# Performance work log

Measured on AMD Instinct MI355X. Metric: run time of the kernel, lower is better.

Reference implementation:

```python
import jax, jax.numpy as jnp
import numpy as np

N = 524288
L, T, F = 24, 1 << 19, 2          # levels, hashmap size per level, features per level
BASE_RES, MAX_RES = 16, 2048
PRIMES = np.array([1, 2654435761, 805459861], dtype=np.uint32)
# per-level resolutions, geometric growth (instant-ngp)
_b = np.exp((np.log(MAX_RES) - np.log(BASE_RES)) / (L - 1))
RES = np.floor(BASE_RES * _b ** np.arange(L)).astype(np.float32)  # [L]
CORNERS = np.stack(np.meshgrid(*[[0, 1]] * 3, indexing='ij'), -1).reshape(8, 3)  # [8,3]


def hash_encode(points, table):
    # points in [-1,1]^3 (bb_sides=2.0) -> [0,1]^3
    x = (points + 1.0) * 0.5
    pos = x[:, None, :] * jnp.asarray(RES)[None, :, None]      # [N,L,3]
    pos0 = jnp.floor(pos)
    w = pos - pos0                                             # [N,L,3] trilinear weights
    c = pos0[:, :, None, :].astype(jnp.uint32) + jnp.asarray(CORNERS, jnp.uint32)[None, None]  # [N,L,8,3]
    p = jnp.asarray(PRIMES)
    idx = ((c[..., 0] * p[0]) ^ (c[..., 1] * p[1]) ^ (c[..., 2] * p[2])) & jnp.uint32(T - 1)   # [N,L,8]
    feats = table[jnp.arange(L)[None, :, None], idx]           # [N,L,8,F]
    cb = jnp.asarray(CORNERS, jnp.float32)[None, None]         # [1,1,8,3]
    wts = jnp.prod(cb * w[:, :, None, :] + (1.0 - cb) * (1.0 - w[:, :, None, :]), axis=-1)  # [N,L,8]
    out = jnp.sum(feats * wts[..., None], axis=2)              # [N,L,F]
    return out.reshape(points.shape[0], L * F)                 # [N,48]


def sh3_encode(d):
    # real spherical harmonics, degree 3 -> 9 coefficients
    x, y, z = d[:, 0], d[:, 1], d[:, 2]
    return jnp.stack([
        jnp.full_like(x, 0.28209479177387814),
        -0.48860251190291987 * y,
        0.48860251190291987 * z,
        -0.48860251190291987 * x,
        1.0925484305920792 * x * y,
        -1.0925484305920792 * y * z,
        0.31539156525252005 * (3.0 * z * z - 1.0),
        -1.0925484305920792 * x * z,
        0.5462742152960396 * (x * x - y * y),
    ], axis=-1)                                                # [N,9]


def _gelu(x):
    return jax.nn.gelu(x, approximate=False)


def reference(samples_3d, samples_dirs, hash_table,
              fw0, fb0, fw1, fb1, fw2, fb2, fw3, fb3,
              rw0, rb0, rw1, rb1, rw2, rb2, iter_nr):
    enc = hash_encode(samples_3d, hash_table)                  # [N,48]
    dirs_enc = jax.lax.stop_gradient(sh3_encode(samples_dirs)) # no-grad dir encoding
    # mlp_feat_and_density: 48->64->64->64->65, GELU hidden, last linear
    h = _gelu(enc @ fw0 + fb0)
    h = _gelu(h @ fw1 + fb1)
    h = _gelu(h @ fw2 + fb2)
    fad = h @ fw3 + fb3                                        # [N,65]
    density = jax.nn.softplus(fad[:, 0:1])                     # [N,1]
    feat_rgb = _gelu(fad[:, 1:65])                             # [N,64]
    x = jnp.concatenate([feat_rgb, dirs_enc], axis=1)          # [N,73]
    # mlp_rgb: 73->64->64->3, GELU hidden, last linear
    h = _gelu(x @ rw0 + rb0)
    h = _gelu(h @ rw1 + rb1)
    rgb = jax.nn.sigmoid(h @ rw2 + rb2)                        # [N,3]
    return rgb, density


def setup_inputs():
    key = jax.random.key(0)
    ks = jax.random.split(key, 24)
    pts = jax.random.uniform(ks[0], (N, 3), minval=-1.0, maxval=1.0)
    d = jax.random.normal(ks[1], (N, 3))
    d = d / jnp.linalg.norm(d, axis=-1, keepdims=True)
    table = jax.random.uniform(ks[2], (L, T, F), minval=-1e-4, maxval=1e-4)

    def lin(k, fi, fo):
        k1, k2 = jax.random.split(k)
        s = 1.0 / np.sqrt(fi)
        return (jax.random.uniform(k1, (fi, fo), minval=-s, maxval=s),
                jax.random.uniform(k2, (fo,), minval=-s, maxval=s))

    inp = {"samples_3d": pts, "samples_dirs": d, "hash_table": table}
    i = 3
    for j, (fi, fo) in enumerate([(48, 64), (64, 64), (64, 64), (64, 65)]):
        w, b = lin(ks[i], fi, fo); inp[f"fw{j}"] = w; inp[f"fb{j}"] = b; i += 1
    for j, (fi, fo) in enumerate([(73, 64), (64, 64), (64, 3)]):
        w, b = lin(ks[i], fi, fo); inp[f"rw{j}"] = w; inp[f"rb{j}"] = b; i += 1
    inp["iter_nr"] = 0
    return inp
```

## Files before the change

### kernel.cpp

```cpp
#include <hip/hip_runtime.h>
#include <math.h>

#define LVL 24
#define TMASK ((1u << 19) - 1u)

typedef short short8 __attribute__((ext_vector_type(8)));
typedef float floatx4 __attribute__((ext_vector_type(4)));

struct ResParams { float r[LVL]; };

__device__ __forceinline__ float bf2f(unsigned short b) {
  union { unsigned u; float f; } t; t.u = ((unsigned)b) << 16; return t.f;
}
__device__ __forceinline__ unsigned f2bf(float f) {
  union { float f; unsigned u; } t; t.f = f;
  unsigned u = t.u;
  u += 0x7FFFu + ((u >> 16) & 1u);
  return u >> 16;
}
__device__ __forceinline__ float geluf(float x) {
  float a = fabsf(x) * 0.7071067811865476f;
  float t = __builtin_amdgcn_rcpf(fmaf(0.3275911f, a, 1.0f));
  float p = fmaf(t, 1.061405429f, -1.453152027f);
  p = fmaf(t, p, 1.421413741f);
  p = fmaf(t, p, -0.284496736f);
  p = fmaf(t, p, 0.254829592f);
  float er = 1.0f - p * t * __expf(-a * a);
  return 0.5f * x * (1.0f + copysignf(er, x));
}
__device__ __forceinline__ floatx4 mfma16(short8 a, short8 b, floatx4 c) {
  return __builtin_amdgcn_mfma_f32_16x16x32_bf16(a, b, c, 0, 0, 0);
}

#define L0_W 0
#define L1_W 4096
#define L2_W 8192
#define L3_W 12288
#define L4_W 17408
#define L5_W 23552
#define L6_W 27648
#define L0_F 0
#define L1_F 512
#define L2_F 1024
#define L3_F 1536
#define L4_F 2176
#define L5_F 2944
#define L6_F 3456

__device__ void prepF(const float* w, short* dst, int K, int NOUT, int KCH, int CBS) {
  int total = KCH * CBS * 64 * 8;
  for (int i = threadIdx.x; i < total; i += 256) {
    int j = i & 7;
    int lane = (i >> 3) & 63;
    int cbc = i >> 9;
    int cb = cbc % CBS;
    int c  = cbc / CBS;
    int n = cb * 16 + (lane & 15);
    int k = c * 32 + (lane >> 4) * 8 + j;
    short v = 0;
    if (k < K && n < NOUT) v = (short)f2bf(w[k * NOUT + n]);
    dst[i] = v;
  }
}
__global__ __launch_bounds__(256) void prep_all(
    const float* __restrict__ fw0, const float* __restrict__ fb0,
    const float* __restrict__ fw1, const float* __restrict__ fb1,
    const float* __restrict__ fw2, const float* __restrict__ fb2,
    const float* __restrict__ fw3, const float* __restrict__ fb3,
    const float* __restrict__ rw0, const float* __restrict__ rb0,
    const float* __restrict__ rw1, const float* __restrict__ rb1,
    const float* __restrict__ rw2, const float* __restrict__ rb2,
    short* __restrict__ Wimg, float* __restrict__ Bimg,
    const float* __restrict__ tbl, unsigned* __restrict__ tblq, int nent,
    int pack_on)
{
  int b = blockIdx.x, tid = threadIdx.x;
  if (b >= 8) {
    if (!pack_on) return;
    int g = (b - 8) * 256 + tid;
    int stride = (gridDim.x - 8) * 256;
    const float4* t4 = (const float4*)tbl;
    uint2* q2 = (uint2*)tblq;
    int n4 = nent >> 1;
    for (int e = g; e < n4; e += stride) {
      float4 v = t4[e];
      uint2 o;
      o.x = f2bf(v.x) | (f2bf(v.y) << 16);
      o.y = f2bf(v.z) | (f2bf(v.w) << 16);
      q2[e] = o;
    }
    return;
  }
  switch (b) {
    case 0: prepF(fw0, Wimg + L0_W, 48, 64, 2, 4); break;
    case 1: prepF(fw1, Wimg + L1_W, 64, 64, 2, 4); break;
    case 2: prepF(fw2, Wimg + L2_W, 64, 64, 2, 4); break;
    case 3: prepF(fw3, Wimg + L3_W, 64, 65, 2, 5); break;
    case 4: prepF(rw0, Wimg + L4_W, 73, 64, 3, 4); break;
    case 5: prepF(rw1, Wimg + L5_W, 64, 64, 2, 4); break;
    case 6: prepF(rw2, Wimg + L6_W, 64,  3, 2, 1); break;
    case 7:
      if (tid < 64) {
        Bimg[tid]       = fb0[tid];
        Bimg[64 + tid]  = fb1[tid];
        Bimg[128 + tid] = fb2[tid];
        Bimg[272 + tid] = rb0[tid];
        Bimg[336 + tid] = rb1[tid];
      }
      if (tid < 80) Bimg[192 + tid] = (tid < 65) ? fb3[tid] : 0.0f;
      if (tid < 16) Bimg[400 + tid] = (tid < 3) ? rb2[tid] : 0.0f;
      break;
  }
}

template<bool PACKED>
__global__ __launch_bounds__(256) void hash_encode_k(
    const float* __restrict__ pts, const float* __restrict__ tbl,
    const unsigned* __restrict__ tblq, unsigned* __restrict__ enc2,
    int N, ResParams rp)
{
  __shared__ float pbuf[4][192];
  int bid  = blockIdx.x;
  int wave = threadIdx.x >> 6;
  int lane = threadIdx.x & 63;
  int l    = bid >> 11;
  int p0   = ((bid & 2047) << 8) + wave * 64;
  int p    = p0 + lane;
  float res = rp.r[l];

  {
    const float* pf = pts + (size_t)p0 * 3;
    pbuf[wave][lane]       = pf[lane];
    pbuf[wave][64 + lane]  = pf[64 + lane];
    pbuf[wave][128 + lane] = pf[128 + lane];
  }
  float x = (pbuf[wave][lane * 3 + 0] + 1.0f) * 0.5f * res;
  float y = (pbuf[wave][lane * 3 + 1] + 1.0f) * 0.5f * res;
  float z = (pbuf[wave][lane * 3 + 2] + 1.0f) * 0.5f * res;

  float fx = floorf(x), fy = floorf(y), fz = floorf(z);
  float w0 = x - fx, w1 = y - fy, w2 = z - fz;
  unsigned c0 = (unsigned)fx, c1 = (unsigned)fy, c2 = (unsigned)fz;
  unsigned hy0 = c1 * 2654435761u, hy1 = hy0 + 2654435761u;
  unsigned hz0 = c2 * 805459861u,  hz1 = hz0 + 805459861u;
  bool ceven = ((c0 & 1u) == 0u);

  const unsigned* tq = PACKED ? (tblq + ((size_t)l << 19)) : nullptr;
  const float*    tf = PACKED ? nullptr : (tbl + ((size_t)l << 20));

  float f0 = 0.f, f1 = 0.f;
  #pragma unroll
  for (int yz = 0; yz < 4; ++yz) {
    unsigned hyz = ((yz & 2) ? hy1 : hy0) ^ ((yz & 1) ? hz1 : hz0);
    float wyz = ((yz & 2) ? w1 : 1.f - w1) * ((yz & 1) ? w2 : 1.f - w2);
    unsigned h0 = (c0 ^ hyz) & TMASK;
    unsigned h1 = ((c0 + 1u) ^ hyz) & TMASK;
    float e00, e01, e10, e11;
    if constexpr (PACKED) {
      unsigned v0, v1;
      if (ceven) {
        uint2 v = *(const uint2*)(tq + (h0 & ~1u));
        v0 = (h0 & 1u) ? v.y : v.x;
        v1 = (h0 & 1u) ? v.x : v.y;
      } else {
        v0 = tq[h0];
        v1 = tq[h1];
      }
      e00 = bf2f((unsigned short)(v0 & 0xffffu)); e01 = bf2f((unsigned short)(v0 >> 16));
      e10 = bf2f((unsigned short)(v1 & 0xffffu)); e11 = bf2f((unsigned short)(v1 >> 16));
    } else {
      if (ceven) {
        float4 v = *(const float4*)(tf + 2u * (h0 & ~1u));
        if (h0 & 1u) { e00 = v.z; e01 = v.w; e10 = v.x; e11 = v.y; }
        else         { e00 = v.x; e01 = v.y; e10 = v.z; e11 = v.w; }
      } else {
        float2 a = *(const float2*)(tf + 2u * h0);
        float2 b = *(const float2*)(tf + 2u * h1);
        e00 = a.x; e01 = a.y; e10 = b.x; e11 = b.y;
      }
    }
    float wa = (1.f - w0) * wyz, wb = w0 * wyz;
    f0 += wa * e00 + wb * e10;
    f1 += wa * e01 + wb * e11;
  }
  enc2[l * N + p] = f2bf(f0) | (f2bf(f1) << 16);
}

template<int NF>
__device__ __forceinline__ void loadB(const short8* Wf, int lane, short8* B) {
  #pragma unroll
  for (int i = 0; i < NF; ++i) B[i] = Wf[i * 64 + lane];
}
template<int KCH, int CBS>
__device__ __forceinline__ void mfma_layer(const short* At, const short8* B,
                                           int m, int quad,
                                           floatx4* acc0, floatx4* acc1) {
  #pragma unroll
  for (int cb = 0; cb < CBS; ++cb) {
    acc0[cb] = (floatx4){0.f, 0.f, 0.f, 0.f};
    acc1[cb] = (floatx4){0.f, 0.f, 0.f, 0.f};
  }
  #pragma unroll
  for (int c = 0; c < KCH; ++c) {
    short8 a0 = *(const short8*)(At + m * 104 + c * 32 + quad * 8);
    short8 a1 = *(const short8*)(At + (16 + m) * 104 + c * 32 + quad * 8);
    #pragma unroll
    for (int cb = 0; cb < CBS; ++cb) {
      acc0[cb] = mfma16(a0, B[c * CBS + cb], acc0[cb]);
      acc1[cb] = mfma16(a1, B[c * CBS + cb], acc1[cb]);
    }
  }
}

__global__ __launch_bounds__(256, 4) void mlp_g(
    const float* __restrict__ dirs,
    const unsigned* __restrict__ enc2,
    const short* __restrict__ Wimg, const float* __restrict__ Bimg,
    float* __restrict__ outp, int Nrows)
{
  __shared__ __align__(16) short Atile[4 * 32 * 104];
  __shared__ __align__(16) float Blds[416];

  const int tid  = threadIdx.x;
  const int wave = tid >> 6;
  const int lane = tid & 63;
  const int m    = lane & 15;
  const int quad = lane >> 4;
  const int row0 = blockIdx.x * 128 + wave * 32;
  short* At = Atile + wave * (32 * 104);
  const short8* Wf = (const short8*)Wimg;

  short8 B[12];
  loadB<8>(Wf + L0_F, lane, B);

  if (tid < 104) ((float4*)Blds)[tid] = ((const float4*)Bimg)[tid];

  if (lane < 32) {
    int row = row0 + lane;
    float dx = dirs[row * 3 + 0];
    float dy = dirs[row * 3 + 1];
    float dz = dirs[row * 3 + 2];
    short8 z8 = {0, 0, 0, 0, 0, 0, 0, 0};
    short8 s07;
    s07[0] = (short)f2bf(0.28209479177387814f);
    s07[1] = (short)f2bf(-0.48860251190291987f * dy);
    s07[2] = (short)f2bf(0.48860251190291987f * dz);
    s07[3] = (short)f2bf(-0.48860251190291987f * dx);
    s07[4] = (short)f2bf(1.0925484305920792f * dx * dy);
    s07[5] = (short)f2bf(-1.0925484305920792f * dy * dz);
    s07[6] = (short)f2bf(0.31539156525252005f * (3.0f * dz * dz - 1.0f));
    s07[7] = (short)f2bf(-1.0925484305920792f * dx * dz);
    short8 s8v = {0, 0, 0, 0, 0, 0, 0, 0};
    s8v[0] = (short)f2bf(0.5462742152960396f * (dx * dx - dy * dy));
    short* rb = At + lane * 104;
    *(short8*)(rb + 48) = z8;
    *(short8*)(rb + 56) = z8;
    *(short8*)(rb + 64) = s07;
    *(short8*)(rb + 72) = s8v;
    *(short8*)(rb + 80) = z8;
    *(short8*)(rb + 88) = z8;
    *(short8*)(rb + 96) = z8;
  }

  for (int i = lane; i < 32 * LVL; i += 64) {
    int l = i >> 5;
    int r = i & 31;
    unsigned v = enc2[l * Nrows + row0 + r];
    *(unsigned*)(At + r * 104 + 2 * l) = v;
  }

  __syncthreads();

  floatx4 acc0[5], acc1[5];

#define EPI_GELU(BOFF)                                                        \
  _Pragma("unroll")                                                           \
  for (int cb = 0; cb < 4; ++cb) {                                            \
    float bc = Blds[(BOFF) + cb * 16 + m];                                    \
    _Pragma("unroll")                                                         \
    for (int r = 0; r < 4; ++r) {                                             \
      At[(quad * 4 + r) * 104 + cb * 16 + m]      = (short)f2bf(geluf(acc0[cb][r] + bc)); \
      At[(16 + quad * 4 + r) * 104 + cb * 16 + m] = (short)f2bf(geluf(acc1[cb][r] + bc)); \
    }                                                                         \
  }

  mfma_layer<2, 4>(At, B, m, quad, acc0, acc1);
  loadB<8>(Wf + L1_F, lane, B);
  EPI_GELU(0)
  mfma_layer<2, 4>(At, B, m, quad, acc0, acc1);
  loadB<8>(Wf + L2_F, lane, B);
  EPI_GELU(64)
  mfma_layer<2, 4>(At, B, m, quad, acc0, acc1);
  loadB<10>(Wf + L3_F, lane, B);
  EPI_GELU(128)
  mfma_layer<2, 5>(At, B, m, quad, acc0, acc1);
  loadB<12>(Wf + L4_F, lane, B);
  #pragma unroll
  for (int cb = 0; cb < 5; ++cb) {
    int col = cb * 16 + m;
    float bc = Blds[192 + col];
    #pragma unroll
    for (int r = 0; r < 4; ++r) {
      #pragma unroll
      for (int t = 0; t < 2; ++t) {
        float v = (t ? acc1[cb][r] : acc0[cb][r]) + bc;
        int row = t * 16 + quad * 4 + r;
        if (col == 0) {
          float d = (v > 15.f) ? v : __logf(1.0f + __expf(v));
          outp[3 * Nrows + row0 + row] = d;
        } else if (col <= 64) {
          At[row * 104 + (col - 1)] = (short)f2bf(geluf(v));
        }
      }
    }
  }
  mfma_layer<3, 4>(At, B, m, quad, acc0, acc1);
  loadB<8>(Wf + L5_F, lane, B);
  EPI_GELU(272)
  mfma_layer<2, 4>(At, B, m, quad, acc0, acc1);
  loadB<2>(Wf + L6_F, lane, B);
  EPI_GELU(336)
  mfma_layer<2, 1>(At, B, m, quad, acc0, acc1);
  {
    float bc = Blds[400 + m];
    #pragma unroll
    for (int r = 0; r < 4; ++r) {
      #pragma unroll
      for (int t = 0; t < 2; ++t) {
        float v = (t ? acc1[0][r] : acc0[0][r]) + bc;
        float s = __builtin_amdgcn_rcpf(1.0f + __expf(-v));
        int row = t * 16 + quad * 4 + r;
        if (m < 3) outp[(row0 + row) * 3 + m] = s;
      }
    }
  }
#undef EPI_GELU
}

#define W0_OFF 0
#define W1_OFF 4608
#define W2_OFF 9216
#define W3_OFF 13824
#define R0_OFF 0
#define R1_OFF 6656
#define R2_OFF 11264

template<int K, int NOUT, int NROWS, int STRIDE>
__device__ void stageW(const float* w, short* dst, int tid) {
  for (int i = tid; i < NROWS * STRIDE; i += 256) {
    int n = i / STRIDE;
    int k = i - n * STRIDE;
    short v = 0;
    if (n < NOUT && k < K) v = (short)f2bf(w[k * NOUT + n]);
    dst[i] = v;
  }
}
template<int NOUT, int NPAD>
__device__ void stageB(const float* b, float* dst, int tid) {
  for (int i = tid; i < NPAD; i += 256) dst[i] = (i < NOUT) ? b[i] : 0.0f;
}
template<int KCH, int CBS, int WSTRIDE>
__device__ __forceinline__ void run_layer(const short* At, const short* Wb,
                                          int m, int quad, floatx4* acc) {
  #pragma unroll
  for (int cb = 0; cb < CBS; ++cb) acc[cb] = (floatx4){0.f, 0.f, 0.f, 0.f};
  #pragma unroll
  for (int c = 0; c < KCH; ++c) {
    short8 a = *(const short8*)(At + m * 104 + c * 32 + quad * 8);
    #pragma unroll
    for (int cb = 0; cb < CBS; ++cb) {
      short8 b = *(const short8*)(Wb + (cb * 16 + m) * WSTRIDE + c * 32 + quad * 8);
      acc[cb] = mfma16(a, b, acc[cb]);
    }
  }
}

__global__ __launch_bounds__(256, 2) void nerf_fused(
    const float* __restrict__ pts,
    const float* __restrict__ dirs,
    const float* __restrict__ tbl,
    const float* __restrict__ fw0, const float* __restrict__ fb0,
    const float* __restrict__ fw1, const float* __restrict__ fb1,
    const float* __restrict__ fw2, const float* __restrict__ fb2,
    const float* __restrict__ fw3, const float* __restrict__ fb3,
    const float* __restrict__ rw0, const float* __restrict__ rb0,
    const float* __restrict__ rw1, const float* __restrict__ rb1,
    const float* __restrict__ rw2, const float* __restrict__ rb2,
    float* __restrict__ outp, int Nrows, ResParams rp)
{
  __shared__ __align__(16) short Wlds[19584];
  __shared__ __align__(16) float Blds[272];
  __shared__ __align__(16) short Atile[4 * 16 * 104];

  const int tid  = threadIdx.x;
  const int wave = tid >> 6;
  const int lane = tid & 63;
  const int m    = lane & 15;
  const int quad = lane >> 4;
  const int row0 = blockIdx.x * 64 + wave * 16;
  short* At = Atile + wave * (16 * 104);

  stageW<48, 64, 64, 72>(fw0, Wlds + W0_OFF, tid);
  stageW<64, 64, 64, 72>(fw1, Wlds + W1_OFF, tid);
  stageW<64, 64, 64, 72>(fw2, Wlds + W2_OFF, tid);
  stageW<64, 65, 80, 72>(fw3, Wlds + W3_OFF, tid);
  stageB<64, 64>(fb0, Blds + 0,   tid);
  stageB<64, 64>(fb1, Blds + 64,  tid);
  stageB<64, 64>(fb2, Blds + 128, tid);
  stageB<65, 80>(fb3, Blds + 192, tid);

  if (lane < 16) {
    int row = row0 + lane;
    float dx = dirs[row * 3 + 0];
    float dy = dirs[row * 3 + 1];
    float dz = dirs[row * 3 + 2];
    short8 z8 = {0, 0, 0, 0, 0, 0, 0, 0};
    short8 s07;
    s07[0] = (short)f2bf(0.28209479177387814f);
    s07[1] = (short)f2bf(-0.48860251190291987f * dy);
    s07[2] = (short)f2bf(0.48860251190291987f * dz);
    s07[3] = (short)f2bf(-0.48860251190291987f * dx);
    s07[4] = (short)f2bf(1.0925484305920792f * dx * dy);
    s07[5] = (short)f2bf(-1.0925484305920792f * dy * dz);
    s07[6] = (short)f2bf(0.31539156525252005f * (3.0f * dz * dz - 1.0f));
    s07[7] = (short)f2bf(-1.0925484305920792f * dx * dz);
    short8 s8v = {0, 0, 0, 0, 0, 0, 0, 0};
    s8v[0] = (short)f2bf(0.5462742152960396f * (dx * dx - dy * dy));
    short* rb = At + lane * 104;
    *(short8*)(rb + 48) = z8;
    *(short8*)(rb + 56) = z8;
    *(short8*)(rb + 64) = s07;
    *(short8*)(rb + 72) = s8v;
    *(short8*)(rb + 80) = z8;
    *(short8*)(rb + 88) = z8;
    *(short8*)(rb + 96) = z8;
  }

  for (int t = lane; t < 16 * LVL; t += 64) {
    int r = t / LVL;
    int l = t - r * LVL;
    int row = row0 + r;
    float res = rp.r[l];
    float x = (pts[row * 3 + 0] + 1.0f) * 0.5f * res;
    float y = (pts[row * 3 + 1] + 1.0f) * 0.5f * res;
    float z = (pts[row * 3 + 2] + 1.0f) * 0.5f * res;
    float fx = floorf(x), fy = floorf(y), fz = floorf(z);
    float w0 = x - fx, w1 = y - fy, w2 = z - fz;
    unsigned c0 = (unsigned)fx, c1 = (unsigned)fy, c2 = (unsigned)fz;
    unsigned ha0 = c0, hb0 = c0 + 1u;
    unsigned ha1 = c1 * 2654435761u, hb1 = ha1 + 2654435761u;
    unsigned ha2 = c2 * 805459861u,  hb2 = ha2 + 805459861u;
    const float* tb = tbl + ((size_t)l << 20);
    float f0 = 0.f, f1 = 0.f;
    #pragma unroll
    for (int i = 0; i < 8; ++i) {
      unsigned h = ((i & 4) ? hb0 : ha0) ^ ((i & 2) ? hb1 : ha1) ^ ((i & 1) ? hb2 : ha2);
      float wt = ((i & 4) ? w0 : 1.f - w0) * ((i & 2) ? w1 : 1.f - w1) * ((i & 1) ? w2 : 1.f - w2);
      float2 fv = *(const float2*)(tb + 2u * (h & TMASK));
      f0 += wt * fv.x;
      f1 += wt * fv.y;
    }
    unsigned pk = f2bf(f0) | (f2bf(f1) << 16);
    *(unsigned*)(At + r * 104 + 2 * l) = pk;
  }

  __syncthreads();

  floatx4 acc[5];

  run_layer<2, 4, 72>(At, Wlds + W0_OFF, m, quad, acc);
  #pragma unroll
  for (int cb = 0; cb < 4; ++cb) {
    float bc = Blds[0 + cb * 16 + m];
    #pragma unroll
    for (int r = 0; r < 4; ++r) {
      float v = geluf(acc[cb][r] + bc);
      At[(quad * 4 + r) * 104 + cb * 16 + m] = (short)f2bf(v);
    }
  }
  run_layer<2, 4, 72>(At, Wlds + W1_OFF, m, quad, acc);
  #pragma unroll
  for (int cb = 0; cb < 4; ++cb) {
    float bc = Blds[64 + cb * 16 + m];
    #pragma unroll
    for (int r = 0; r < 4; ++r) {
      float v = geluf(acc[cb][r] + bc);
      At[(quad * 4 + r) * 104 + cb * 16 + m] = (short)f2bf(v);
    }
  }
  run_layer<2, 4, 72>(At, Wlds + W2_OFF, m, quad, acc);
  #pragma unroll
  for (int cb = 0; cb < 4; ++cb) {
    float bc = Blds[128 + cb * 16 + m];
    #pragma unroll
    for (int r = 0; r < 4; ++r) {
      float v = geluf(acc[cb][r] + bc);
      At[(quad * 4 + r) * 104 + cb * 16 + m] = (short)f2bf(v);
    }
  }
  run_layer<2, 5, 72>(At, Wlds + W3_OFF, m, quad, acc);
  #pragma unroll
  for (int cb = 0; cb < 5; ++cb) {
    int col = cb * 16 + m;
    float bc = Blds[192 + col];
    #pragma unroll
    for (int r = 0; r < 4; ++r) {
      float v = acc[cb][r] + bc;
      int row = quad * 4 + r;
      if (col == 0) {
        float d = (v > 15.f) ? v : __logf(1.0f + __expf(v));
        outp[3 * Nrows + row0 + row] = d;
      } else if (col <= 64) {
        At[row * 104 + (col - 1)] = (short)f2bf(geluf(v));
      }
    }
  }

  __syncthreads();

  stageW<73, 64, 64, 104>(rw0, Wlds + R0_OFF, tid);
  stageW<64, 64, 64,  72>(rw1, Wlds + R1_OFF, tid);
  stageW<64,  3, 16,  72>(rw2, Wlds + R2_OFF, tid);
  stageB<64, 64>(rb0, Blds + 0,   tid);
  stageB<64, 64>(rb1, Blds + 64,  tid);
  stageB< 3, 16>(rb2, Blds + 128, tid);

  __syncthreads();

  run_layer<3, 4, 104>(At, Wlds + R0_OFF, m, quad, acc);
  #pragma unroll
  for (int cb = 0; cb < 4; ++cb) {
    float bc = Blds[0 + cb * 16 + m];
    #pragma unroll
    for (int r = 0; r < 4; ++r) {
      float v = geluf(acc[cb][r] + bc);
      At[(quad * 4 + r) * 104 + cb * 16 + m] = (short)f2bf(v);
    }
  }
  run_layer<2, 4, 72>(At, Wlds + R1_OFF, m, quad, acc);
  #pragma unroll
  for (int cb = 0; cb < 4; ++cb) {
    float bc = Blds[64 + cb * 16 + m];
    #pragma unroll
    for (int r = 0; r < 4; ++r) {
      float v = geluf(acc[cb][r] + bc);
      At[(quad * 4 + r) * 104 + cb * 16 + m] = (short)f2bf(v);
    }
  }
  run_layer<2, 1, 72>(At, Wlds + R2_OFF, m, quad, acc);
  {
    float bc = Blds[128 + m];
    #pragma unroll
    for (int r = 0; r < 4; ++r) {
      float v = acc[0][r] + bc;
      float s = __builtin_amdgcn_rcpf(1.0f + __expf(-v));
      if (m < 3) outp[(row0 + quad * 4 + r) * 3 + m] = s;
    }
  }
}

extern "C" void kernel_launch(void* const* d_in, const int* in_sizes, int n_in,
                              void* d_out, int out_size, void* d_ws, size_t ws_size,
                              hipStream_t stream) {
  ResParams rp;
  double b = exp((log(2048.0) - log(16.0)) / 23.0);
  for (int l = 0; l < LVL; ++l) rp.r[l] = (float)floor(16.0 * pow(b, (double)l));

  const float* pts  = (const float*)d_in[0];
  const float* dirs = (const float*)d_in[1];
  const float* tbl  = (const float*)d_in[2];
  float* outp = (float*)d_out;

  int n = in_sizes[0] / 3;
  int nent = LVL << 19;
  size_t enc_b = (size_t)LVL * (size_t)n * 4u;
  size_t img_reserve = 65536;
  size_t tbl_b = (size_t)nent * 4u;
  size_t full_need = enc_b + img_reserve + tbl_b;
  size_t mid_need  = enc_b + img_reserve;

  unsigned* enc2 = (unsigned*)d_ws;
  short* Wimg = (short*)((char*)d_ws + enc_b);
  float* Bimg = (float*)((char*)d_ws + enc_b + 57344);
  unsigned* tblq = (unsigned*)((char*)d_ws + enc_b + img_reserve);
  int enc_blocks = LVL * (n / 256);
  int mlp_blocks = n / 128;

  if (ws_size >= full_need) {
    prep_all<<<8 + 6144, 256, 0, stream>>>(
        (const float*)d_in[3],  (const float*)d_in[4],
        (const float*)d_in[5],  (const float*)d_in[6],
        (const float*)d_in[7],  (const float*)d_in[8],
        (const float*)d_in[9],  (const float*)d_in[10],
        (const float*)d_in[11], (const float*)d_in[12],
        (const float*)d_in[13], (const float*)d_in[14],
        (const float*)d_in[15], (const float*)d_in[16],
        Wimg, Bimg, tbl, tblq, nent, 1);
    hash_encode_k<true><<<enc_blocks, 256, 0, stream>>>(pts, tbl, tblq, enc2, n, rp);
    mlp_g<<<mlp_blocks, 256, 0, stream>>>(dirs, enc2, Wimg, Bimg, outp, n);
  } else if (ws_size >= mid_need) {
    prep_all<<<8, 256, 0, stream>>>(
        (const float*)d_in[3],  (const float*)d_in[4],
        (const float*)d_in[5],  (const float*)d_in[6],
        (const float*)d_in[7],  (const float*)d_in[8],
        (const float*)d_in[9],  (const float*)d_in[10],
        (const float*)d_in[11], (const float*)d_in[12],
        (const float*)d_in[13], (const float*)d_in[14],
        (const float*)d_in[15], (const float*)d_in[16],
        Wimg, Bimg, tbl, nullptr, nent, 0);
    hash_encode_k<false><<<enc_blocks, 256, 0, stream>>>(pts, tbl, nullptr, enc2, n, rp);
    mlp_g<<<mlp_blocks, 256, 0, stream>>>(dirs, enc2, Wimg, Bimg, outp, n);
  } else {
    nerf_fused<<<n / 64, 256, 0, stream>>>(
        pts, dirs, tbl,
        (const float*)d_in[3],  (const float*)d_in[4],
        (const float*)d_in[5],  (const float*)d_in[6],
        (const float*)d_in[7],  (const float*)d_in[8],
        (const float*)d_in[9],  (const float*)d_in[10],
        (const float*)d_in[11], (const float*)d_in[12],
        (const float*)d_in[13], (const float*)d_in[14],
        (const float*)d_in[15], (const float*)d_in[16],
        outp, n, rp);
  }
}
```

Measured before the change: 526.2 us.

## Fuse hash encoding into MLP kernel, dropping the encoding intermediate buffer

Merges the separate hash-encode kernel into the MLP kernel: each wave computes the 24-level hash features for its 32 rows directly into the LDS tile, with two levels handled per iteration across the half-waves. This removes the global write and read of the [24,N] bf16 encoding buffer and one kernel launch. MLP weights are now loaded from global or cache per MFMA step instead of being held in registers, which lowers register pressure but adds load latency inside the matmul loops. Gather locality changes too: the old kernel processed one level per block, keeping that level's table slice hot in cache, while the fused kernel touches all levels per block.

```diff
diff --git a/kernel.cpp b/kernel.cpp
--- a/kernel.cpp
+++ b/kernel.cpp
@@ -113,88 +113,10 @@
   }
 }
 
-template<bool PACKED>
-__global__ __launch_bounds__(256) void hash_encode_k(
-    const float* __restrict__ pts, const float* __restrict__ tbl,
-    const unsigned* __restrict__ tblq, unsigned* __restrict__ enc2,
-    int N, ResParams rp)
-{
-  __shared__ float pbuf[4][192];
-  int bid  = blockIdx.x;
-  int wave = threadIdx.x >> 6;
-  int lane = threadIdx.x & 63;
-  int l    = bid >> 11;
-  int p0   = ((bid & 2047) << 8) + wave * 64;
-  int p    = p0 + lane;
-  float res = rp.r[l];
-
-  {
-    const float* pf = pts + (size_t)p0 * 3;
-    pbuf[wave][lane]       = pf[lane];
-    pbuf[wave][64 + lane]  = pf[64 + lane];
-    pbuf[wave][128 + lane] = pf[128 + lane];
-  }
-  float x = (pbuf[wave][lane * 3 + 0] + 1.0f) * 0.5f * res;
-  float y = (pbuf[wave][lane * 3 + 1] + 1.0f) * 0.5f * res;
-  float z = (pbuf[wave][lane * 3 + 2] + 1.0f) * 0.5f * res;
-
-  float fx = floorf(x), fy = floorf(y), fz = floorf(z);
-  float w0 = x - fx, w1 = y - fy, w2 = z - fz;
-  unsigned c0 = (unsigned)fx, c1 = (unsigned)fy, c2 = (unsigned)fz;
-  unsigned hy0 = c1 * 2654435761u, hy1 = hy0 + 2654435761u;
-  unsigned hz0 = c2 * 805459861u,  hz1 = hz0 + 805459861u;
-  bool ceven = ((c0 & 1u) == 0u);
-
-  const unsigned* tq = PACKED ? (tblq + ((size_t)l << 19)) : nullptr;
-  const float*    tf = PACKED ? nullptr : (tbl + ((size_t)l << 20));
-
-  float f0 = 0.f, f1 = 0.f;
-  #pragma unroll
-  for (int yz = 0; yz < 4; ++yz) {
-    unsigned hyz = ((yz & 2) ? hy1 : hy0) ^ ((yz & 1) ? hz1 : hz0);
-    float wyz = ((yz & 2) ? w1 : 1.f - w1) * ((yz & 1) ? w2 : 1.f - w2);
-    unsigned h0 = (c0 ^ hyz) & TMASK;
-    unsigned h1 = ((c0 + 1u) ^ hyz) & TMASK;
-    float e00, e01, e10, e11;
-    if constexpr (PACKED) {
-      unsigned v0, v1;
-      if (ceven) {
-        uint2 v = *(const uint2*)(tq + (h0 & ~1u));
-        v0 = (h0 & 1u) ? v.y : v.x;
-        v1 = (h0 & 1u) ? v.x : v.y;
-      } else {
-        v0 = tq[h0];
-        v1 = tq[h1];
-      }
-      e00 = bf2f((unsigned short)(v0 & 0xffffu)); e01 = bf2f((unsigned short)(v0 >> 16));
-      e10 = bf2f((unsigned short)(v1 & 0xffffu)); e11 = bf2f((unsigned short)(v1 >> 16));
-    } else {
-      if (ceven) {
-        float4 v = *(const float4*)(tf + 2u * (h0 & ~1u));
-        if (h0 & 1u) { e00 = v.z; e01 = v.w; e10 = v.x; e11 = v.y; }
-        else         { e00 = v.x; e01 = v.y; e10 = v.z; e11 = v.w; }
-      } else {
-        float2 a = *(const float2*)(tf + 2u * h0);
-        float2 b = *(const float2*)(tf + 2u * h1);
-        e00 = a.x; e01 = a.y; e10 = b.x; e11 = b.y;
-      }
-    }
-    float wa = (1.f - w0) * wyz, wb = w0 * wyz;
-    f0 += wa * e00 + wb * e10;
-    f1 += wa * e01 + wb * e11;
-  }
-  enc2[l * N + p] = f2bf(f0) | (f2bf(f1) << 16);
-}
-
-template<int NF>
-__device__ __forceinline__ void loadB(const short8* Wf, int lane, short8* B) {
-  #pragma unroll
-  for (int i = 0; i < NF; ++i) B[i] = Wf[i * 64 + lane];
-}
 template<int KCH, int CBS>
-__device__ __forceinline__ void mfma_layer(const short* At, const short8* B,
-                                           int m, int quad,
-                                           floatx4* acc0, floatx4* acc1) {
+__device__ __forceinline__ void run_layer32(const short* At, const short8* Wf,
+                                            int lane, int m, int quad,
+                                            floatx4* acc0, floatx4* acc1) {
   #pragma unroll
   for (int cb = 0; cb < CBS; ++cb) {
     acc0[cb] = (floatx4){0.f, 0.f, 0.f, 0.f};
@@ -206,20 +128,23 @@
     short8 a1 = *(const short8*)(At + (16 + m) * 104 + c * 32 + quad * 8);
     #pragma unroll
     for (int cb = 0; cb < CBS; ++cb) {
-      acc0[cb] = mfma16(a0, B[c * CBS + cb], acc0[cb]);
-      acc1[cb] = mfma16(a1, B[c * CBS + cb], acc1[cb]);
-    }
-  }
-}
-
-__global__ __launch_bounds__(256, 4) void mlp_g(
-    const float* __restrict__ dirs,
-    const unsigned* __restrict__ enc2,
+      short8 b = Wf[(c * CBS + cb) * 64 + lane];
+      acc0[cb] = mfma16(a0, b, acc0[cb]);
+      acc1[cb] = mfma16(a1, b, acc1[cb]);
+    }
+  }
+}
+
+template<bool PACKED>
+__global__ __launch_bounds__(256, 4) void nerf_block(
+    const float* __restrict__ pts, const float* __restrict__ dirs,
+    const float* __restrict__ tblf, const unsigned* __restrict__ tblq,
     const short* __restrict__ Wimg, const float* __restrict__ Bimg,
-    float* __restrict__ outp, int Nrows)
+    float* __restrict__ outp, int Nrows, ResParams rp)
 {
   __shared__ __align__(16) short Atile[4 * 32 * 104];
   __shared__ __align__(16) float Blds[416];
+  __shared__ float pbuf[4][96];
 
   const int tid  = threadIdx.x;
   const int wave = tid >> 6;
@@ -230,10 +155,13 @@
   short* At = Atile + wave * (32 * 104);
   const short8* Wf = (const short8*)Wimg;
 
-  short8 B[12];
-  loadB<8>(Wf + L0_F, lane, B);
-
   if (tid < 104) ((float4*)Blds)[tid] = ((const float4*)Bimg)[tid];
+
+  {
+    const float* pf = pts + (size_t)row0 * 3;
+    pbuf[wave][lane] = pf[lane];
+    if (lane < 32) pbuf[wave][64 + lane] = pf[64 + lane];
+  }
 
   if (lane < 32) {
     int row = row0 + lane;
@@ -262,11 +190,64 @@
     *(short8*)(rb + 96) = z8;
   }
 
-  for (int i = lane; i < 32 * LVL; i += 64) {
-    int l = i >> 5;
-    int r = i & 31;
-    unsigned v = enc2[l * Nrows + row0 + r];
-    *(unsigned*)(At + r * 104 + 2 * l) = v;
+  {
+    const int r = lane & 31;
+    const float px = pbuf[wave][r * 3 + 0];
+    const float py = pbuf[wave][r * 3 + 1];
+    const float pz = pbuf[wave][r * 3 + 2];
+    #pragma unroll
+    for (int it = 0; it < 12; ++it) {
+      const int l = 2 * it + (lane >> 5);
+      float res = (lane & 32) ? rp.r[2 * it + 1] : rp.r[2 * it];
+      float x = (px + 1.0f) * 0.5f * res;
+      float y = (py + 1.0f) * 0.5f * res;
+      float z = (pz + 1.0f) * 0.5f * res;
+      float fx = floorf(x), fy = floorf(y), fz = floorf(z);
+      float w0 = x - fx, w1 = y - fy, w2 = z - fz;
+      unsigned c0 = (unsigned)fx, c1 = (unsigned)fy, c2 = (unsigned)fz;
+      unsigned hy0 = c1 * 2654435761u, hy1 = hy0 + 2654435761u;
+      unsigned hz0 = c2 * 805459861u,  hz1 = hz0 + 805459861u;
+      bool ceven = ((c0 & 1u) == 0u);
+      unsigned lbase = (unsigned)l << 19;
+
+      float f0 = 0.f, f1 = 0.f;
+      #pragma unroll
+      for (int yz = 0; yz < 4; ++yz) {
+        unsigned hyz = ((yz & 2) ? hy1 : hy0) ^ ((yz & 1) ? hz1 : hz0);
+        float wyz = ((yz & 2) ? w1 : 1.f - w1) * ((yz & 1) ? w2 : 1.f - w2);
+        unsigned h0 = (c0 ^ hyz) & TMASK;
+        unsigned h1 = ((c0 + 1u) ^ hyz) & TMASK;
+        float e00, e01, e10, e11;
+        if constexpr (PACKED) {
+          unsigned v0, v1;
+          if (ceven) {
+            uint2 v = *(const uint2*)(tblq + (size_t)(lbase | (h0 & ~1u)));
+            v0 = (h0 & 1u) ? v.y : v.x;
+            v1 = (h0 & 1u) ? v.x : v.y;
+          } else {
+            v0 = tblq[(size_t)(lbase | h0)];
+            v1 = tblq[(size_t)(lbase | h1)];
+          }
+          e00 = bf2f((unsigned short)(v0 & 0xffffu)); e01 = bf2f((unsigned short)(v0 >> 16));
+          e10 = bf2f((unsigned short)(v1 & 0xffffu)); e11 = bf2f((unsigned short)(v1 >> 16));
+        } else {
+          const float* tf = tblf + ((size_t)l << 20);
+          if (ceven) {
+            float4 v = *(const float4*)(tf + 2u * (h0 & ~1u));
+            if (h0 & 1u) { e00 = v.z; e01 = v.w; e10 = v.x; e11 = v.y; }
+            else         { e00 = v.x; e01 = v.y; e10 = v.z; e11 = v.w; }
+          } else {
+            float2 a = *(const float2*)(tf + 2u * h0);
+            float2 b = *(const float2*)(tf + 2u * h1);
+            e00 = a.x; e01 = a.y; e10 = b.x; e11 = b.y;
+          }
+        }
+        float wa = (1.f - w0) * wyz, wb = w0 * wyz;
+        f0 += wa * e00 + wb * e10;
+        f1 += wa * e01 + wb * e11;
+      }
+      *(unsigned*)(At + r * 104 + 2 * l) = f2bf(f0) | (f2bf(f1) << 16);
+    }
   }
 
   __syncthreads();
@@ -284,17 +265,13 @@
     }                                                                         \
   }
 
-  mfma_layer<2, 4>(At, B, m, quad, acc0, acc1);
-  loadB<8>(Wf + L1_F, lane, B);
+  run_layer32<2, 4>(At, Wf + L0_F, lane, m, quad, acc0, acc1);
   EPI_GELU(0)
-  mfma_layer<2, 4>(At, B, m, quad, acc0, acc1);
-  loadB<8>(Wf + L2_F, lane, B);
+  run_layer32<2, 4>(At, Wf + L1_F, lane, m, quad, acc0, acc1);
   EPI_GELU(64)
-  mfma_layer<2, 4>(At, B, m, quad, acc0, acc1);
-  loadB<10>(Wf + L3_F, lane, B);
+  run_layer32<2, 4>(At, Wf + L2_F, lane, m, quad, acc0, acc1);
   EPI_GELU(128)
-  mfma_layer<2, 5>(At, B, m, quad, acc0, acc1);
-  loadB<12>(Wf + L4_F, lane, B);
+  run_layer32<2, 5>(At, Wf + L3_F, lane, m, quad, acc0, acc1);
   #pragma unroll
   for (int cb = 0; cb < 5; ++cb) {
     int col = cb * 16 + m;
@@ -314,13 +291,11 @@
       }
     }
   }
-  mfma_layer<3, 4>(At, B, m, quad, acc0, acc1);
-  loadB<8>(Wf + L5_F, lane, B);
+  run_layer32<3, 4>(At, Wf + L4_F, lane, m, quad, acc0, acc1);
   EPI_GELU(272)
-  mfma_layer<2, 4>(At, B, m, quad, acc0, acc1);
-  loadB<2>(Wf + L6_F, lane, B);
+  run_layer32<2, 4>(At, Wf + L5_F, lane, m, quad, acc0, acc1);
   EPI_GELU(336)
-  mfma_layer<2, 1>(At, B, m, quad, acc0, acc1);
+  run_layer32<2, 1>(At, Wf + L6_F, lane, m, quad, acc0, acc1);
   {
     float bc = Blds[400 + m];
     #pragma unroll
@@ -573,18 +548,14 @@
 
   int n = in_sizes[0] / 3;
   int nent = LVL << 19;
-  size_t enc_b = (size_t)LVL * (size_t)n * 4u;
   size_t img_reserve = 65536;
   size_t tbl_b = (size_t)nent * 4u;
-  size_t full_need = enc_b + img_reserve + tbl_b;
-  size_t mid_need  = enc_b + img_reserve;
-
-  unsigned* enc2 = (unsigned*)d_ws;
-  short* Wimg = (short*)((char*)d_ws + enc_b);
-  float* Bimg = (float*)((char*)d_ws + enc_b + 57344);
-  unsigned* tblq = (unsigned*)((char*)d_ws + enc_b + img_reserve);
-  int enc_blocks = LVL * (n / 256);
-  int mlp_blocks = n / 128;
+  size_t full_need = img_reserve + tbl_b;
+
+  short* Wimg = (short*)d_ws;
+  float* Bimg = (float*)((char*)d_ws + 57344);
+  unsigned* tblq = (unsigned*)((char*)d_ws + img_reserve);
+  int blocks = n / 128;
 
   if (ws_size >= full_need) {
     prep_all<<<8 + 6144, 256, 0, stream>>>(
@@ -596,9 +567,9 @@
         (const float*)d_in[13], (const float*)d_in[14],
         (const float*)d_in[15], (const float*)d_in[16],
         Wimg, Bimg, tbl, tblq, nent, 1);
-    hash_encode_k<true><<<enc_blocks, 256, 0, stream>>>(pts, tbl, tblq, enc2, n, rp);
-    mlp_g<<<mlp_blocks, 256, 0, stream>>>(dirs, enc2, Wimg, Bimg, outp, n);
-  } else if (ws_size >= mid_need) {
+    nerf_block<true><<<blocks, 256, 0, stream>>>(
+        pts, dirs, tbl, tblq, Wimg, Bimg, outp, n, rp);
+  } else if (ws_size >= img_reserve) {
     prep_all<<<8, 256, 0, stream>>>(
         (const float*)d_in[3],  (const float*)d_in[4],
         (const float*)d_in[5],  (const float*)d_in[6],
@@ -608,8 +579,8 @@
         (const float*)d_in[13], (const float*)d_in[14],
         (const float*)d_in[15], (const float*)d_in[16],
         Wimg, Bimg, tbl, nullptr, nent, 0);
-    hash_encode_k<false><<<enc_blocks, 256, 0, stream>>>(pts, tbl, nullptr, enc2, n, rp);
-    mlp_g<<<mlp_blocks, 256, 0, stream>>>(dirs, enc2, Wimg, Bimg, outp, n);
+    nerf_block<false><<<blocks, 256, 0, stream>>>(
+        pts, dirs, tbl, nullptr, Wimg, Bimg, outp, n, rp);
   } else {
     nerf_fused<<<n / 64, 256, 0, stream>>>(
         pts, dirs, tbl,
```

Result: slower. 684.2 us (+30.0%).
